# Optimization experiments

Measured on AMD Instinct MI355X. Metric: run time of the kernel, lower is better.

Reference implementation:

```python
import jax, jax.numpy as jnp
import numpy as np

B, S, T, C, H = 16, 64, 4096, 512, 8
D = C // H
NEG = jnp.float32(-1e30)


def setup_inputs() -> dict:
    key = jax.random.key(0)
    ks = jax.random.split(key, 12)
    x = jax.random.normal(ks[0], (1, C, 1), dtype=jnp.float32)
    eh = jax.random.normal(ks[1], (B, C, T), dtype=jnp.float32)
    # ragged shot boundaries -> fixed (B, S) start/end arrays, end > start
    bounds = jnp.sort(jax.random.randint(ks[2], (B, S + 1), 0, T), axis=-1)
    shot_starts = bounds[:, :-1].astype(jnp.int32)
    shot_ends = jnp.maximum(bounds[:, 1:], shot_starts + 1).astype(jnp.int32)
    sc = 1.0 / np.sqrt(C)
    Wq = jax.random.normal(ks[3], (C, C), dtype=jnp.float32) * sc
    bq = jnp.zeros((C,), dtype=jnp.float32)
    Wk = jax.random.normal(ks[4], (C, C), dtype=jnp.float32) * sc
    bk = jnp.zeros((C,), dtype=jnp.float32)
    Wv = jax.random.normal(ks[5], (C, C), dtype=jnp.float32) * sc
    bv = jnp.zeros((C,), dtype=jnp.float32)
    Wp = jax.random.normal(ks[6], (C, C), dtype=jnp.float32) * sc
    bp = jnp.zeros((C,), dtype=jnp.float32)
    return {"x": x, "encoder_hidden_states": eh, "shot_starts": shot_starts,
            "shot_ends": shot_ends, "Wq": Wq, "bq": bq, "Wk": Wk, "bk": bk,
            "Wv": Wv, "bv": bv, "Wp": Wp, "bp": bp}


def reference(x, encoder_hidden_states, shot_starts, shot_ends,
              Wq, bq, Wk, bk, Wv, bv, Wp, bp):
    scale = 1.0 / np.sqrt(D)
    # 1x1 conv == pointwise matmul over channels
    q = (Wq @ x[0] + bq[:, None])            # (C, 1)
    k = jnp.einsum('oc,bct->bot', Wk, encoder_hidden_states) + bk[None, :, None]
    v = jnp.einsum('oc,bct->bot', Wv, encoder_hidden_states) + bv[None, :, None]
    qh = q.reshape(H, D) * scale             # (H, D) single query per head
    kh = k.reshape(B, H, D, T)               # (B, H, D, T)
    vh = v.reshape(B, H, D, T).transpose(0, 1, 3, 2)  # (B, H, T, D)
    att = jnp.einsum('hd,bhdt->bht', qh, kh)          # (B, H, T)
    pos = jnp.arange(T)
    seg = (pos[None, None, :] >= shot_starts[:, :, None]) & \
          (pos[None, None, :] < shot_ends[:, :, None])  # (B, S, T)
    logits = jnp.where(seg[:, :, None, :], att[:, None, :, :], NEG)  # (B,S,H,T)
    p = jax.nn.softmax(logits, axis=-1)
    out = jnp.einsum('bsht,bhtd->bshd', p, vh)        # (B, S, H, D)
    out = out.reshape(B * S, C)
    out = out @ Wp.T + bp                              # proj (1x1 conv)
    return out[:, :, None]                             # (B*S, C, 1)
```

## Files before the change

kernel.cpp:

```cpp
#include <hip/hip_runtime.h>
#include <cstdint>
#include <cstddef>

#define B_ 16
#define S_ 64
#define T_ 4096
#define C_ 512
#define H_ 8

#define WS_QKT     0
#define WS_QB      4096
#define WS_QH      4104
#define WS_MS      4616
#define WS_LI      12808
#define WS_CNT     21000
#define WS_CSEG    21016
#define WS_CIDX    23064
#define WS_CMUL    25112
#define WS_ATT     28672
#define WS_WSUM    552960
#define WS_ATTNOUT 4747264

__global__ void k_prep1(const float* __restrict__ x, const float* __restrict__ Wq,
                        const float* __restrict__ bq, float* __restrict__ qh_g) {
  __shared__ float xs[C_];
  __shared__ float red[256];
  int tid = threadIdx.x;
  xs[tid] = x[tid];
  xs[tid + 256] = x[tid + 256];
  __syncthreads();
  int r0 = blockIdx.x * 32;
  int rl = tid >> 3, sub = tid & 7;
  int r = r0 + rl;
  const float* wr = Wq + (size_t)r * C_ + sub * 64;
  const float* xp = xs + sub * 64;
  float s = 0.f;
#pragma unroll
  for (int i = 0; i < 64; i += 4) {
    float4 w = *(const float4*)(wr + i);
    s += w.x * xp[i] + w.y * xp[i + 1] + w.z * xp[i + 2] + w.w * xp[i + 3];
  }
  red[tid] = s;
  __syncthreads();
  if (sub == 0) {
    float tot = bq[r];
#pragma unroll
    for (int i = 0; i < 8; ++i) tot += red[rl * 8 + i];
    qh_g[r] = tot * 0.125f;
  }
}

__global__ void k_prep2(const float* __restrict__ qh_g,
                        const float* __restrict__ Wk,
                        const float* __restrict__ bk, float* __restrict__ qkT,
                        float* __restrict__ qb) {
  __shared__ float qhs[64];
  int tid = threadIdx.x;
  int h = blockIdx.x;
  if (tid < 64) qhs[tid] = qh_g[h * 64 + tid];
  __syncthreads();
  int c0 = tid, c1 = tid + 256;
  float s0 = 0.f, s1 = 0.f;
#pragma unroll 8
  for (int d = 0; d < 64; ++d) {
    const float* row = Wk + (size_t)(h * 64 + d) * C_;
    float q = qhs[d];
    s0 += q * row[c0];
    s1 += q * row[c1];
  }
  qkT[c0 * 8 + h] = s0;
  qkT[c1 * 8 + h] = s1;
  if (tid < 64) {
    float w = qhs[tid] * bk[h * 64 + tid];
#pragma unroll
    for (int off = 32; off > 0; off >>= 1) w += __shfl_down(w, off, 64);
    if (tid == 0) qb[h] = w;
  }
}

__global__ __launch_bounds__(256, 4) void k_att(
    const float* __restrict__ eh, const float* __restrict__ qkT,
    const float* __restrict__ qb, float* __restrict__ att) {
  __shared__ float qks[C_ * 8];
  __shared__ float part[4 * 8 * 64];
  int tid = threadIdx.x;
  int tl = tid & 63, cg = tid >> 6;
  int b = blockIdx.y;
  int t0 = blockIdx.x * 64;
#pragma unroll
  for (int i = 0; i < 16; ++i) qks[tid + i * 256] = qkT[tid + i * 256];
  __syncthreads();
  const float* ehp = eh + ((size_t)b * C_ + (size_t)cg * 128) * T_ + t0 + tl;
  float acc[8];
#pragma unroll
  for (int h = 0; h < 8; ++h) acc[h] = 0.f;
#pragma unroll 4
  for (int j = 0; j < 128; ++j) {
    float e = ehp[(size_t)j * T_];
    const float4 q0 = *(const float4*)&qks[(cg * 128 + j) * 8];
    const float4 q1 = *(const float4*)&qks[(cg * 128 + j) * 8 + 4];
    acc[0] += q0.x * e; acc[1] += q0.y * e; acc[2] += q0.z * e; acc[3] += q0.w * e;
    acc[4] += q1.x * e; acc[5] += q1.y * e; acc[6] += q1.z * e; acc[7] += q1.w * e;
  }
#pragma unroll
  for (int h = 0; h < 8; ++h) part[(cg * 8 + h) * 64 + tl] = acc[h];
  __syncthreads();
#pragma unroll
  for (int i = 0; i < 2; ++i) {
    int idx = tid + i * 256;
    int h = idx >> 6, tt = idx & 63;
    float v = part[(0 * 8 + h) * 64 + tt] + part[(1 * 8 + h) * 64 + tt] +
              part[(2 * 8 + h) * 64 + tt] + part[(3 * 8 + h) * 64 + tt] + qb[h];
    att[((size_t)b * H_ + h) * T_ + t0 + tt] = v;
  }
}

__global__ void k_stats(const float* __restrict__ att,
                        const int* __restrict__ starts,
                        const int* __restrict__ ends, float* __restrict__ ms,
                        float* __restrict__ li) {
  int tid = threadIdx.x;
  int n = blockIdx.x;
  int b = n >> 6;
  int start = starts[n], end = ends[n];
  int h = tid >> 5, tl = tid & 31;
  const float* ah = att + ((size_t)b * H_ + h) * T_;
  float mloc = -3.0e38f;
  for (int t = start + tl; t < end; t += 32) mloc = fmaxf(mloc, ah[t]);
#pragma unroll
  for (int off = 16; off > 0; off >>= 1)
    mloc = fmaxf(mloc, __shfl_xor(mloc, off, 32));
  float lloc = 0.f;
  for (int t = start + tl; t < end; t += 32) lloc += __expf(ah[t] - mloc);
#pragma unroll
  for (int off = 16; off > 0; off >>= 1) lloc += __shfl_xor(lloc, off, 32);
  if (tl == 0) { ms[n * 8 + h] = mloc; li[n * 8 + h] = 1.f / lloc; }
}

__global__ void k_map(const int* __restrict__ starts,
                      const int* __restrict__ ends, int* __restrict__ cnt,
                      int* __restrict__ cseg, int* __restrict__ cidx,
                      int* __restrict__ cmul) {
  int b = blockIdx.x;
  int s = threadIdx.x;
  int st = starts[b * 64 + s], en = ends[b * 64 + s];
  int cbase = st & ~31;
  int nch = (en - cbase + 127) >> 7;
  int x = nch;
#pragma unroll
  for (int off = 1; off < 64; off <<= 1) {
    int y = __shfl_up(x, off, 64);
    if (s >= off) x += y;
  }
  int pre = x - nch;
  for (int k = 0; k < nch; ++k) {
    cseg[b * 128 + pre + k] = s;
    cidx[b * 128 + pre + k] = k;
    cmul[b * 128 + pre + k] = (nch > 1) ? 1 : 0;
  }
  if (s == 63) cnt[b] = x;
}

__global__ __launch_bounds__(256, 4) void k_wsum(
    const float* __restrict__ eh, const float* __restrict__ att,
    const float* __restrict__ ms, const float* __restrict__ li,
    const int* __restrict__ starts, const int* __restrict__ ends,
    const int* __restrict__ cnt, const int* __restrict__ cseg,
    const int* __restrict__ cidx, const int* __restrict__ cmul,
    float* __restrict__ wsum) {
  __shared__ float pl[8 * 136];
  int b = blockIdx.y;
  int i = blockIdx.x;
  if (i >= cnt[b]) return;
  int tid = threadIdx.x;
  int s = cseg[b * 128 + i];
  int k = cidx[b * 128 + i];
  int mul = cmul[b * 128 + i];
  int n = b * 64 + s;
  int st = starts[n], en = ends[n];
  int cbase = st & ~31;
  int t_lo = cbase + k * 128;
  if (st > t_lo) t_lo = st;
  int t_hi = cbase + (k + 1) * 128;
  if (en < t_hi) t_hi = en;
  int base = t_lo & ~3;

  int h = tid >> 5, l32 = tid & 31;
  float msn = ms[n * 8 + h], lin = li[n * 8 + h];
  const float* ah = att + ((size_t)b * H_ + h) * T_;
  for (int j = l32; j < 136; j += 32) {
    int t = base + j;
    float pv = 0.f;
    if (t >= t_lo && t < t_hi) pv = __expf(ah[t] - msn) * lin;
    pl[h * 136 + j] = pv;
  }
  __syncthreads();

  float acc0[8], acc1[8];
#pragma unroll
  for (int hh = 0; hh < 8; ++hh) { acc0[hh] = 0.f; acc1[hh] = 0.f; }
  const float* e0p = eh + ((size_t)b * C_ + tid) * T_ + base;
  const float* e1p = e0p + (size_t)256 * T_;
  int jmax = t_hi - base;
  int jv = jmax & ~3;
#pragma unroll 2
  for (int j = 0; j < jv; j += 4) {
    float4 e0 = *(const float4*)(e0p + j);
    float4 e1 = *(const float4*)(e1p + j);
#pragma unroll
    for (int hh = 0; hh < 8; ++hh) {
      const float4 p = *(const float4*)&pl[hh * 136 + j];
      acc0[hh] += p.x * e0.x + p.y * e0.y + p.z * e0.z + p.w * e0.w;
      acc1[hh] += p.x * e1.x + p.y * e1.y + p.z * e1.z + p.w * e1.w;
    }
  }
  for (int j = jv; j < jmax; ++j) {
    float e0 = e0p[j], e1 = e1p[j];
#pragma unroll
    for (int hh = 0; hh < 8; ++hh) {
      float p = pl[hh * 136 + j];
      acc0[hh] += p * e0;
      acc1[hh] += p * e1;
    }
  }
  float* wp = wsum + (size_t)n * (H_ * C_);
  if (!mul) {
#pragma unroll
    for (int hh = 0; hh < 8; ++hh) {
      wp[hh * C_ + tid] = acc0[hh];
      wp[hh * C_ + 256 + tid] = acc1[hh];
    }
  } else {
#pragma unroll
    for (int hh = 0; hh < 8; ++hh) {
      atomicAdd(&wp[hh * C_ + tid], acc0[hh]);
      atomicAdd(&wp[hh * C_ + 256 + tid], acc1[hh]);
    }
  }
}

__global__ __launch_bounds__(256, 4) void k_gemm(
    const float* __restrict__ A, long aRow, long aColPerY,
    const float* __restrict__ Bm, const float* __restrict__ bias,
    float* __restrict__ Cc) {
  __shared__ float As[32 * 36];
  __shared__ float Bs[64 * 36];
  int tid = threadIdx.x;
  int n0 = blockIdx.x * 32;
  int y = blockIdx.y;
  const float* Abase = A + (size_t)n0 * aRow + (size_t)y * aColPerY;
  const float* Bbase = Bm + (size_t)(y * 64) * C_;
  int tx = tid & 15, ty = tid >> 4;
  float acc[2][4];
#pragma unroll
  for (int a = 0; a < 2; ++a)
#pragma unroll
    for (int bb = 0; bb < 4; ++bb) acc[a][bb] = 0.f;
  for (int k0 = 0; k0 < 512; k0 += 32) {
#pragma unroll
    for (int i = 0; i < 4; ++i) {
      int idx = tid + i * 256;
      int r = idx >> 5, cc = idx & 31;
      As[r * 36 + cc] = Abase[(size_t)r * aRow + k0 + cc];
    }
#pragma unroll
    for (int i = 0; i < 8; ++i) {
      int idx = tid + i * 256;
      int r = idx >> 5, cc = idx & 31;
      Bs[r * 36 + cc] = Bbase[(size_t)r * C_ + k0 + cc];
    }
    __syncthreads();
#pragma unroll
    for (int k = 0; k < 32; k += 4) {
      const float4 a0 = *(const float4*)&As[(ty * 2 + 0) * 36 + k];
      const float4 a1 = *(const float4*)&As[(ty * 2 + 1) * 36 + k];
#pragma unroll
      for (int bb = 0; bb < 4; ++bb) {
        const float4 bv = *(const float4*)&Bs[(tx * 4 + bb) * 36 + k];
        acc[0][bb] += a0.x * bv.x + a0.y * bv.y + a0.z * bv.z + a0.w * bv.w;
        acc[1][bb] += a1.x * bv.x + a1.y * bv.y + a1.z * bv.z + a1.w * bv.w;
      }
    }
    __syncthreads();
  }
#pragma unroll
  for (int a = 0; a < 2; ++a) {
    int nn = n0 + ty * 2 + a;
    float4 o;
    o.x = acc[a][0] + bias[y * 64 + tx * 4 + 0];
    o.y = acc[a][1] + bias[y * 64 + tx * 4 + 1];
    o.z = acc[a][2] + bias[y * 64 + tx * 4 + 2];
    o.w = acc[a][3] + bias[y * 64 + tx * 4 + 3];
    *(float4*)&Cc[(size_t)nn * C_ + y * 64 + tx * 4] = o;
  }
}

extern "C" void kernel_launch(void* const* d_in, const int* in_sizes, int n_in,
                              void* d_out, int out_size, void* d_ws,
                              size_t ws_size, hipStream_t stream) {
  const float* x = (const float*)d_in[0];
  const float* eh = (const float*)d_in[1];
  const int* shot_starts = (const int*)d_in[2];
  const int* shot_ends = (const int*)d_in[3];
  const float* Wq = (const float*)d_in[4];
  const float* bq = (const float*)d_in[5];
  const float* Wk = (const float*)d_in[6];
  const float* bk = (const float*)d_in[7];
  const float* Wv = (const float*)d_in[8];
  const float* bv = (const float*)d_in[9];
  const float* Wp = (const float*)d_in[10];
  const float* bp = (const float*)d_in[11];
  float* out = (float*)d_out;

  float* ws = (float*)d_ws;
  float* qkT = ws + WS_QKT;
  float* qb = ws + WS_QB;
  float* qh = ws + WS_QH;
  float* ms = ws + WS_MS;
  float* li = ws + WS_LI;
  int* cnt = (int*)(ws + WS_CNT);
  int* cseg = (int*)(ws + WS_CSEG);
  int* cidx = (int*)(ws + WS_CIDX);
  int* cmul = (int*)(ws + WS_CMUL);
  float* att = ws + WS_ATT;
  float* wsum = ws + WS_WSUM;
  float* attnout = ws + WS_ATTNOUT;

  hipMemsetAsync(wsum, 0, (size_t)1024 * H_ * C_ * sizeof(float), stream);
  k_prep1<<<16, 256, 0, stream>>>(x, Wq, bq, qh);
  k_prep2<<<8, 256, 0, stream>>>(qh, Wk, bk, qkT, qb);
  k_att<<<dim3(T_ / 64, B_), 256, 0, stream>>>(eh, qkT, qb, att);
  k_stats<<<B_ * S_, 256, 0, stream>>>(att, shot_starts, shot_ends, ms, li);
  k_map<<<B_, 64, 0, stream>>>(shot_starts, shot_ends, cnt, cseg, cidx, cmul);
  k_wsum<<<dim3(128, B_), 256, 0, stream>>>(eh, att, ms, li, shot_starts,
                                            shot_ends, cnt, cseg, cidx, cmul,
                                            wsum);
  k_gemm<<<dim3(32, 8), 256, 0, stream>>>(wsum, (long)(H_ * C_), (long)C_, Wv,
                                          bv, attnout);
  k_gemm<<<dim3(32, 8), 256, 0, stream>>>(attnout, (long)C_, 0L, Wp, bp, out);
}
```

Before: 373.9 us.

## Drop softmax stats kernel; defer normalization into V-projection GEMM epilogue

Removes the separate max/sum statistics kernel. Softmax numerators are now computed as exp(logit) without subtracting the max, the per-segment denominator is accumulated with atomics inside the weighted-sum kernel, and the division is applied in the first GEMM's epilogue. The attention-score kernel now writes per-channel-group partial sums instead of reducing them in shared memory, and each thread handles two time positions. The weighted-sum kernel sums those four partials itself and loads eh in 32-wide blocks. Skipping the max subtraction risks overflow for large logits, and it adds extra partial-sum traffic and a second memset.

```diff
diff --git a/kernel.cpp b/kernel.cpp
--- a/kernel.cpp
+++ b/kernel.cpp
@@ -11,15 +11,14 @@
 #define WS_QKT     0
 #define WS_QB      4096
 #define WS_QH      4104
-#define WS_MS      4616
-#define WS_LI      12808
-#define WS_CNT     21000
-#define WS_CSEG    21016
-#define WS_CIDX    23064
-#define WS_CMUL    25112
-#define WS_ATT     28672
-#define WS_WSUM    552960
-#define WS_ATTNOUT 4747264
+#define WS_LG      4616
+#define WS_CNT     12808
+#define WS_CSEG    12824
+#define WS_CIDX    14872
+#define WS_CMUL    16920
+#define WS_APART   18968
+#define WS_WSUM    2116120
+#define WS_ATTNOUT 6310424
 
 __global__ void k_prep1(const float* __restrict__ x, const float* __restrict__ Wq,
                         const float* __restrict__ bq, float* __restrict__ qh_g) {
@@ -78,63 +77,38 @@
   }
 }
 
-__global__ __launch_bounds__(256, 4) void k_att(
+__global__ __launch_bounds__(256, 2) void k_att(
     const float* __restrict__ eh, const float* __restrict__ qkT,
-    const float* __restrict__ qb, float* __restrict__ att) {
+    float* __restrict__ apart) {
   __shared__ float qks[C_ * 8];
-  __shared__ float part[4 * 8 * 64];
   int tid = threadIdx.x;
   int tl = tid & 63, cg = tid >> 6;
   int b = blockIdx.y;
-  int t0 = blockIdx.x * 64;
+  int t0 = blockIdx.x * 128;
 #pragma unroll
   for (int i = 0; i < 16; ++i) qks[tid + i * 256] = qkT[tid + i * 256];
   __syncthreads();
   const float* ehp = eh + ((size_t)b * C_ + (size_t)cg * 128) * T_ + t0 + tl;
-  float acc[8];
-#pragma unroll
-  for (int h = 0; h < 8; ++h) acc[h] = 0.f;
+  float acc0[8], acc1[8];
+#pragma unroll
+  for (int h = 0; h < 8; ++h) { acc0[h] = 0.f; acc1[h] = 0.f; }
 #pragma unroll 4
   for (int j = 0; j < 128; ++j) {
-    float e = ehp[(size_t)j * T_];
+    float e0 = ehp[(size_t)j * T_];
+    float e1 = ehp[(size_t)j * T_ + 64];
     const float4 q0 = *(const float4*)&qks[(cg * 128 + j) * 8];
     const float4 q1 = *(const float4*)&qks[(cg * 128 + j) * 8 + 4];
-    acc[0] += q0.x * e; acc[1] += q0.y * e; acc[2] += q0.z * e; acc[3] += q0.w * e;
-    acc[4] += q1.x * e; acc[5] += q1.y * e; acc[6] += q1.z * e; acc[7] += q1.w * e;
-  }
-#pragma unroll
-  for (int h = 0; h < 8; ++h) part[(cg * 8 + h) * 64 + tl] = acc[h];
-  __syncthreads();
-#pragma unroll
-  for (int i = 0; i < 2; ++i) {
-    int idx = tid + i * 256;
-    int h = idx >> 6, tt = idx & 63;
-    float v = part[(0 * 8 + h) * 64 + tt] + part[(1 * 8 + h) * 64 + tt] +
-              part[(2 * 8 + h) * 64 + tt] + part[(3 * 8 + h) * 64 + tt] + qb[h];
-    att[((size_t)b * H_ + h) * T_ + t0 + tt] = v;
-  }
-}
-
-__global__ void k_stats(const float* __restrict__ att,
-                        const int* __restrict__ starts,
-                        const int* __restrict__ ends, float* __restrict__ ms,
-                        float* __restrict__ li) {
-  int tid = threadIdx.x;
-  int n = blockIdx.x;
-  int b = n >> 6;
-  int start = starts[n], end = ends[n];
-  int h = tid >> 5, tl = tid & 31;
-  const float* ah = att + ((size_t)b * H_ + h) * T_;
-  float mloc = -3.0e38f;
-  for (int t = start + tl; t < end; t += 32) mloc = fmaxf(mloc, ah[t]);
-#pragma unroll
-  for (int off = 16; off > 0; off >>= 1)
-    mloc = fmaxf(mloc, __shfl_xor(mloc, off, 32));
-  float lloc = 0.f;
-  for (int t = start + tl; t < end; t += 32) lloc += __expf(ah[t] - mloc);
-#pragma unroll
-  for (int off = 16; off > 0; off >>= 1) lloc += __shfl_xor(lloc, off, 32);
-  if (tl == 0) { ms[n * 8 + h] = mloc; li[n * 8 + h] = 1.f / lloc; }
+    acc0[0] += q0.x * e0; acc0[1] += q0.y * e0; acc0[2] += q0.z * e0; acc0[3] += q0.w * e0;
+    acc0[4] += q1.x * e0; acc0[5] += q1.y * e0; acc0[6] += q1.z * e0; acc0[7] += q1.w * e0;
+    acc1[0] += q0.x * e1; acc1[1] += q0.y * e1; acc1[2] += q0.z * e1; acc1[3] += q0.w * e1;
+    acc1[4] += q1.x * e1; acc1[5] += q1.y * e1; acc1[6] += q1.z * e1; acc1[7] += q1.w * e1;
+  }
+  float* ap = apart + (((size_t)cg * 16 + b) * 8) * T_ + t0 + tl;
+#pragma unroll
+  for (int h = 0; h < 8; ++h) {
+    ap[(size_t)h * T_] = acc0[h];
+    ap[(size_t)h * T_ + 64] = acc1[h];
+  }
 }
 
 __global__ void k_map(const int* __restrict__ starts,
@@ -161,14 +135,14 @@
   if (s == 63) cnt[b] = x;
 }
 
-__global__ __launch_bounds__(256, 4) void k_wsum(
-    const float* __restrict__ eh, const float* __restrict__ att,
-    const float* __restrict__ ms, const float* __restrict__ li,
-    const int* __restrict__ starts, const int* __restrict__ ends,
-    const int* __restrict__ cnt, const int* __restrict__ cseg,
-    const int* __restrict__ cidx, const int* __restrict__ cmul,
-    float* __restrict__ wsum) {
-  __shared__ float pl[8 * 136];
+__global__ __launch_bounds__(256, 2) void k_wsum(
+    const float* __restrict__ eh, const float* __restrict__ apart,
+    const float* __restrict__ qb, const int* __restrict__ starts,
+    const int* __restrict__ ends, const int* __restrict__ cnt,
+    const int* __restrict__ cseg, const int* __restrict__ cidx,
+    const int* __restrict__ cmul, float* __restrict__ wsum,
+    float* __restrict__ l_g) {
+  __shared__ float pl[8 * 132];
   int b = blockIdx.y;
   int i = blockIdx.x;
   if (i >= cnt[b]) return;
@@ -183,58 +157,77 @@
   if (st > t_lo) t_lo = st;
   int t_hi = cbase + (k + 1) * 128;
   if (en < t_hi) t_hi = en;
-  int base = t_lo & ~3;
-
-  int h = tid >> 5, l32 = tid & 31;
-  float msn = ms[n * 8 + h], lin = li[n * 8 + h];
-  const float* ah = att + ((size_t)b * H_ + h) * T_;
-  for (int j = l32; j < 136; j += 32) {
-    int t = base + j;
+  int base = t_lo & ~31;
+  int span = t_hi - base;
+  int jpad = (span + 31) & ~31;
+
+#pragma unroll
+  for (int r = 0; r < 4; ++r) {
+    int idx = tid + r * 256;
+    int h = idx >> 7, tt = idx & 127;
+    int t = base + tt;
     float pv = 0.f;
-    if (t >= t_lo && t < t_hi) pv = __expf(ah[t] - msn) * lin;
-    pl[h * 136 + j] = pv;
-  }
-  __syncthreads();
+    if (t >= t_lo && t < t_hi) {
+      float a = qb[h];
+      size_t o = ((size_t)b * 8 + h) * T_ + t;
+      a += apart[o];
+      a += apart[o + (size_t)128 * T_];
+      a += apart[o + (size_t)256 * T_];
+      a += apart[o + (size_t)384 * T_];
+      pv = __expf(a);
+    }
+    pl[h * 132 + tt] = pv;
+  }
+  __syncthreads();
+
+  if (tid < 64) {
+    int h = tid >> 3, k8 = tid & 7;
+    float ls = 0.f;
+#pragma unroll
+    for (int q = 0; q < 16; ++q) ls += pl[h * 132 + k8 * 16 + q];
+    ls += __shfl_down(ls, 4, 8);
+    ls += __shfl_down(ls, 2, 8);
+    ls += __shfl_down(ls, 1, 8);
+    if (k8 == 0) atomicAdd(&l_g[n * 8 + h], ls);
+  }
 
   float acc0[8], acc1[8];
 #pragma unroll
-  for (int hh = 0; hh < 8; ++hh) { acc0[hh] = 0.f; acc1[hh] = 0.f; }
+  for (int h = 0; h < 8; ++h) { acc0[h] = 0.f; acc1[h] = 0.f; }
   const float* e0p = eh + ((size_t)b * C_ + tid) * T_ + base;
   const float* e1p = e0p + (size_t)256 * T_;
-  int jmax = t_hi - base;
-  int jv = jmax & ~3;
-#pragma unroll 2
-  for (int j = 0; j < jv; j += 4) {
-    float4 e0 = *(const float4*)(e0p + j);
-    float4 e1 = *(const float4*)(e1p + j);
-#pragma unroll
-    for (int hh = 0; hh < 8; ++hh) {
-      const float4 p = *(const float4*)&pl[hh * 136 + j];
-      acc0[hh] += p.x * e0.x + p.y * e0.y + p.z * e0.z + p.w * e0.w;
-      acc1[hh] += p.x * e1.x + p.y * e1.y + p.z * e1.z + p.w * e1.w;
-    }
-  }
-  for (int j = jv; j < jmax; ++j) {
-    float e0 = e0p[j], e1 = e1p[j];
-#pragma unroll
-    for (int hh = 0; hh < 8; ++hh) {
-      float p = pl[hh * 136 + j];
-      acc0[hh] += p * e0;
-      acc1[hh] += p * e1;
+  int nb = jpad >> 5;
+  for (int jb = 0; jb < nb; ++jb) {
+    int jo = jb * 32;
+    float4 e0f[8], e1f[8];
+#pragma unroll
+    for (int q = 0; q < 8; ++q) e0f[q] = *(const float4*)(e0p + jo + q * 4);
+#pragma unroll
+    for (int q = 0; q < 8; ++q) e1f[q] = *(const float4*)(e1p + jo + q * 4);
+#pragma unroll
+    for (int t4 = 0; t4 < 8; ++t4) {
+#pragma unroll
+      for (int h = 0; h < 8; ++h) {
+        const float4 p = *(const float4*)&pl[h * 132 + jo + t4 * 4];
+        acc0[h] += p.x * e0f[t4].x + p.y * e0f[t4].y + p.z * e0f[t4].z +
+                   p.w * e0f[t4].w;
+        acc1[h] += p.x * e1f[t4].x + p.y * e1f[t4].y + p.z * e1f[t4].z +
+                   p.w * e1f[t4].w;
+      }
     }
   }
   float* wp = wsum + (size_t)n * (H_ * C_);
   if (!mul) {
 #pragma unroll
-    for (int hh = 0; hh < 8; ++hh) {
-      wp[hh * C_ + tid] = acc0[hh];
-      wp[hh * C_ + 256 + tid] = acc1[hh];
+    for (int h = 0; h < 8; ++h) {
+      wp[h * C_ + tid] = acc0[h];
+      wp[h * C_ + 256 + tid] = acc1[h];
     }
   } else {
 #pragma unroll
-    for (int hh = 0; hh < 8; ++hh) {
-      atomicAdd(&wp[hh * C_ + tid], acc0[hh]);
-      atomicAdd(&wp[hh * C_ + 256 + tid], acc1[hh]);
+    for (int h = 0; h < 8; ++h) {
+      atomicAdd(&wp[h * C_ + tid], acc0[h]);
+      atomicAdd(&wp[h * C_ + 256 + tid], acc1[h]);
     }
   }
 }
@@ -242,7 +235,7 @@
 __global__ __launch_bounds__(256, 4) void k_gemm(
     const float* __restrict__ A, long aRow, long aColPerY,
     const float* __restrict__ Bm, const float* __restrict__ bias,
-    float* __restrict__ Cc) {
+    const float* __restrict__ l_g, float* __restrict__ Cc) {
   __shared__ float As[32 * 36];
   __shared__ float Bs[64 * 36];
   int tid = threadIdx.x;
@@ -286,11 +279,12 @@
 #pragma unroll
   for (int a = 0; a < 2; ++a) {
     int nn = n0 + ty * 2 + a;
+    float sc = l_g ? (1.0f / l_g[nn * 8 + y]) : 1.0f;
     float4 o;
-    o.x = acc[a][0] + bias[y * 64 + tx * 4 + 0];
-    o.y = acc[a][1] + bias[y * 64 + tx * 4 + 1];
-    o.z = acc[a][2] + bias[y * 64 + tx * 4 + 2];
-    o.w = acc[a][3] + bias[y * 64 + tx * 4 + 3];
+    o.x = acc[a][0] * sc + bias[y * 64 + tx * 4 + 0];
+    o.y = acc[a][1] * sc + bias[y * 64 + tx * 4 + 1];
+    o.z = acc[a][2] * sc + bias[y * 64 + tx * 4 + 2];
+    o.w = acc[a][3] * sc + bias[y * 64 + tx * 4 + 3];
     *(float4*)&Cc[(size_t)nn * C_ + y * 64 + tx * 4] = o;
   }
 }
@@ -316,26 +310,26 @@
   float* qkT = ws + WS_QKT;
   float* qb = ws + WS_QB;
   float* qh = ws + WS_QH;
-  float* ms = ws + WS_MS;
-  float* li = ws + WS_LI;
+  float* l_g = ws + WS_LG;
   int* cnt = (int*)(ws + WS_CNT);
   int* cseg = (int*)(ws + WS_CSEG);
   int* cidx = (int*)(ws + WS_CIDX);
   int* cmul = (int*)(ws + WS_CMUL);
-  float* att = ws + WS_ATT;
+  float* apart = ws + WS_APART;
   float* wsum = ws + WS_WSUM;
   float* attnout = ws + WS_ATTNOUT;
 
   hipMemsetAsync(wsum, 0, (size_t)1024 * H_ * C_ * sizeof(float), stream);
+  hipMemsetAsync(l_g, 0, (size_t)1024 * H_ * sizeof(float), stream);
   k_prep1<<<16, 256, 0, stream>>>(x, Wq, bq, qh);
   k_prep2<<<8, 256, 0, stream>>>(qh, Wk, bk, qkT, qb);
-  k_att<<<dim3(T_ / 64, B_), 256, 0, stream>>>(eh, qkT, qb, att);
-  k_stats<<<B_ * S_, 256, 0, stream>>>(att, shot_starts, shot_ends, ms, li);
+  k_att<<<dim3(T_ / 128, B_), 256, 0, stream>>>(eh, qkT, apart);
   k_map<<<B_, 64, 0, stream>>>(shot_starts, shot_ends, cnt, cseg, cidx, cmul);
-  k_wsum<<<dim3(128, B_), 256, 0, stream>>>(eh, att, ms, li, shot_starts,
+  k_wsum<<<dim3(128, B_), 256, 0, stream>>>(eh, apart, qb, shot_starts,
                                             shot_ends, cnt, cseg, cidx, cmul,
-                                            wsum);
+                                            wsum, l_g);
   k_gemm<<<dim3(32, 8), 256, 0, stream>>>(wsum, (long)(H_ * C_), (long)C_, Wv,
-                                          bv, attnout);
-  k_gemm<<<dim3(32, 8), 256, 0, stream>>>(attnout, (long)C_, 0L, Wp, bp, out);
-}
+                                          bv, l_g, attnout);
+  k_gemm<<<dim3(32, 8), 256, 0, stream>>>(attnout, (long)C_, 0L, Wp, bp,
+                                          nullptr, out);
+}
```

New measurement: 390.7 us. 4.5% more time.
